# Performance work log

Measured on AMD Instinct MI355X. Metric: run time of the kernel, lower is better.

The kernel has to match this reference:

```python
import jax, jax.numpy as jnp
import numpy as np

B, H, W, C, NH, WS, NB = 8, 64, 64, 384, 12, 8, 2
N = H * W
NWT = WS * WS  # tokens per window
SHIFT = WS // 2

def _rel_index(ws):
    coords = np.stack(np.meshgrid(np.arange(ws), np.arange(ws), indexing='ij')).reshape(2, -1)
    rel = (coords[:, :, None] - coords[:, None, :]).transpose(1, 2, 0)
    rel[..., 0] += ws - 1
    rel[..., 1] += ws - 1
    rel[..., 0] *= 2 * ws - 1
    return rel.sum(-1)  # (ws*ws, ws*ws)

REL_IDX = _rel_index(WS)

def _shift_mask(h, w, ws, shift):
    img = np.zeros((h, w))
    cnt = 0
    for hs in (slice(0, -ws), slice(-ws, -shift), slice(-shift, None)):
        for wsl in (slice(0, -ws), slice(-ws, -shift), slice(-shift, None)):
            img[hs, wsl] = cnt
            cnt += 1
    win = img.reshape(h // ws, ws, w // ws, ws).transpose(0, 2, 1, 3).reshape(-1, ws * ws)
    diff = win[:, None, :] - win[:, :, None]
    return np.where(diff != 0, -100.0, 0.0).astype(np.float32)  # (nW, NWT, NWT)

MASK = jnp.asarray(_shift_mask(H, W, WS, SHIFT))

def _ln(x, g, b, eps=1e-5):
    m = jnp.mean(x, -1, keepdims=True)
    v = jnp.mean((x - m) ** 2, -1, keepdims=True)
    return (x - m) * jax.lax.rsqrt(v + eps) * g + b

def _partition(x):
    b = x.shape[0]
    x = x.reshape(b, H // WS, WS, W // WS, WS, C).transpose(0, 1, 3, 2, 4, 5)
    return x.reshape(-1, NWT, C)

def _reverse(wx, b):
    x = wx.reshape(b, H // WS, W // WS, WS, WS, C).transpose(0, 1, 3, 2, 4, 5)
    return x.reshape(b, H, W, C)

def _attention(xw, qkv_w, qkv_b, proj_w, proj_b, rpb, mask):
    B_, Nt, Cc = xw.shape
    hd = Cc // NH
    qkv = (xw @ qkv_w + qkv_b).reshape(B_, Nt, 3, NH, hd).transpose(2, 0, 3, 1, 4)
    q, k, v = qkv[0], qkv[1], qkv[2]
    bias = rpb[REL_IDX].transpose(2, 0, 1)[None]  # (1, NH, Nt, Nt)
    attn = jnp.einsum('bhnd,bhmd->bhnm', q * (hd ** -0.5), k) + bias
    if mask is not None:
        nW = mask.shape[0]
        attn = attn.reshape(B_ // nW, nW, NH, Nt, Nt) + mask[None, :, None]
        attn = attn.reshape(B_, NH, Nt, Nt)
    attn = jax.nn.softmax(attn, axis=-1)
    out = jnp.einsum('bhnm,bhmd->bhnd', attn, v).transpose(0, 2, 1, 3).reshape(B_, Nt, Cc)
    return out @ proj_w + proj_b

def _swin_block(x, p, shift):
    n1g, n1b, n2g, n2b, qw, qb, pw, pb, w1, b1, w2, b2, rpb = p
    shortcut = x
    h = _ln(x, n1g, n1b)
    if shift > 0:
        h = jnp.roll(h, (-shift, -shift), axis=(1, 2))
    hw = _attention(_partition(h), qw, qb, pw, pb, rpb, MASK if shift > 0 else None)
    h = _reverse(hw, x.shape[0])
    if shift > 0:
        h = jnp.roll(h, (shift, shift), axis=(1, 2))
    x = shortcut + h
    h = _ln(x, n2g, n2b)
    h = jax.nn.gelu(h @ w1 + b1) @ w2 + b2
    return x + h


def setup_inputs() -> dict:
    key = jax.random.key(0)
    ks = jax.random.split(key, 6)
    s = 0.02
    return {
        'x': jax.random.normal(ks[0], (B, N, C), jnp.float32),
        'outer_g': jnp.ones((NB, C), jnp.float32),
        'outer_b': jnp.zeros((NB, C), jnp.float32),
        'n1_g': jnp.ones((NB, C), jnp.float32),
        'n1_b': jnp.zeros((NB, C), jnp.float32),
        'n2_g': jnp.ones((NB, C), jnp.float32),
        'n2_b': jnp.zeros((NB, C), jnp.float32),
        'qkv_w': jax.random.normal(ks[1], (NB, C, 3 * C), jnp.float32) * s,
        'qkv_b': jnp.zeros((NB, 3 * C), jnp.float32),
        'proj_w': jax.random.normal(ks[2], (NB, C, C), jnp.float32) * s,
        'proj_b': jnp.zeros((NB, C), jnp.float32),
        'mlp_w1': jax.random.normal(ks[3], (NB, C, 4 * C), jnp.float32) * s,
        'mlp_b1': jnp.zeros((NB, 4 * C), jnp.float32),
        'mlp_w2': jax.random.normal(ks[4], (NB, 4 * C, C), jnp.float32) * s,
        'mlp_b2': jnp.zeros((NB, C), jnp.float32),
        'rpb': jax.random.normal(ks[5], (NB, (2 * WS - 1) ** 2, NH), jnp.float32) * s,
    }


def reference(x, outer_g, outer_b, n1_g, n1_b, n2_g, n2_b, qkv_w, qkv_b, proj_w, proj_b, mlp_w1, mlp_b1, mlp_w2, mlp_b2, rpb):
    xv = x.reshape(B, H, W, C)
    for i in range(NB):
        shift = 0 if i % 2 == 0 else SHIFT
        p = (n1_g[i], n1_b[i], n2_g[i], n2_b[i], qkv_w[i], qkv_b[i], proj_w[i], proj_b[i],
             mlp_w1[i], mlp_b1[i], mlp_w2[i], mlp_b2[i], rpb[i])
        residual = xv
        xv = _swin_block(_ln(xv, outer_g[i], outer_b[i]), p, shift) + residual
    return xv.reshape(B, N, C)
```

## Files before the change

### kernel.cpp

```cpp
#include <hip/hip_runtime.h>
#include <hip/hip_bf16.h>

#define BATCH 8
#define HDIM 64
#define WDIM 64
#define CC 384
#define NHE 12
#define HD 32
#define NTOK 32768
#define NBLK 2

typedef short short8 __attribute__((ext_vector_type(8)));
typedef float f32x4 __attribute__((ext_vector_type(4)));

__device__ __forceinline__ float bf2f(unsigned short u) {
  return __uint_as_float(((unsigned int)u) << 16);
}
__device__ __forceinline__ unsigned short f2bf(float f) {
  __hip_bfloat16 h = __float2bfloat16(f);
  return *reinterpret_cast<unsigned short*>(&h);
}
__device__ __forceinline__ float wave_sum(float s) {
#pragma unroll
  for (int o = 32; o; o >>= 1) s += __shfl_xor(s, o, 64);
  return s;
}
__device__ __forceinline__ float gelu_f(float x) {
  float y = 0.7978845608028654f * (x + 0.044715f * x * x * x);
  float t = 1.0f - 2.0f / (__expf(2.0f * y) + 1.0f);
  return 0.5f * x * (1.0f + t);
}
__device__ __forceinline__ int regid(int x) {
  return x < 56 ? 0 : (x < 60 ? 1 : 2);
}
__device__ __forceinline__ void gload16(const void* g, void* l) {
  __builtin_amdgcn_global_load_lds(
      (const __attribute__((address_space(1))) unsigned int*)g,
      (__attribute__((address_space(3))) unsigned int*)l, 16, 0, 0);
}

__global__ __launch_bounds__(256) void wconv_all_kernel(
    const float* __restrict__ qkvw, const float* __restrict__ pw,
    const float* __restrict__ w1, const float* __restrict__ w2,
    unsigned short* __restrict__ wt) {
  int t = blockIdx.x;
  const int i = t / 432;
  t -= i * 432;
  unsigned short* wq = wt + (size_t)i * 1769472;
  const float* src;
  unsigned short* dst;
  int K, N, nx;
  if (t < 108)      { src = qkvw + (size_t)i * 442368; dst = wq;           K = 384;  N = 1152; nx = 18; }
  else if (t < 144) { t -= 108; src = pw + (size_t)i * 147456; dst = wq + 442368;  K = 384;  N = 384;  nx = 6; }
  else if (t < 288) { t -= 144; src = w1 + (size_t)i * 589824; dst = wq + 589824;  K = 384;  N = 1536; nx = 24; }
  else              { t -= 288; src = w2 + (size_t)i * 589824; dst = wq + 1179648; K = 1536; N = 384;  nx = 6; }
  const int bn = (t % nx) * 64, bk = (t / nx) * 64;
  __shared__ float tile[64 * 65];
  const int tt = threadIdx.x;
  const int lk = tt >> 2, ln = (tt & 3) * 16;
  const float* ps = src + (size_t)(bk + lk) * N + bn + ln;
#pragma unroll
  for (int j = 0; j < 4; ++j)
    *(float4*)&tile[lk * 65 + ln + 4 * j] = *(const float4*)(ps + 4 * j);
  __syncthreads();
  const int on = tt >> 2, ok = (tt & 3) * 16;
  unsigned short ob[16];
#pragma unroll
  for (int j = 0; j < 16; ++j) ob[j] = f2bf(tile[(ok + j) * 65 + on]);
  uint4* pd = (uint4*)(dst + (size_t)(bn + on) * K + bk + ok);
  pd[0] = ((const uint4*)ob)[0];
  pd[1] = ((const uint4*)ob)[1];
}

__global__ __launch_bounds__(256) void bias_prep_kernel(
    const float* __restrict__ rpb, float* __restrict__ biasT) {
  int idx = blockIdx.x * 256 + threadIdx.x;
  int m = idx & 63;
  int n = (idx >> 6) & 63;
  int h = idx >> 12;
  int dr = (n >> 3) - (m >> 3) + 7;
  int dc = (n & 7) - (m & 7) + 7;
  biasT[idx] = rpb[(dr * 15 + dc) * NHE + h];
}

__global__ __launch_bounds__(256) void ln_fused_kernel(
    const float* __restrict__ xin, const float* __restrict__ og,
    const float* __restrict__ ob, const float* __restrict__ n1g,
    const float* __restrict__ n1b, unsigned short* __restrict__ y0h,
    unsigned short* __restrict__ abuf, int shift) {
  const int lane = threadIdx.x & 63;
  const int token = blockIdx.x * 4 + (threadIdx.x >> 6);
  const float* px = xin + (size_t)token * CC;
  float v[6];
#pragma unroll
  for (int j = 0; j < 6; ++j) v[j] = px[j * 64 + lane];
  float s = 0.f;
#pragma unroll
  for (int j = 0; j < 6; ++j) s += v[j];
  s = wave_sum(s);
  float mean = s * (1.0f / CC);
  float q = 0.f;
#pragma unroll
  for (int j = 0; j < 6; ++j) { float d = v[j] - mean; q += d * d; }
  q = wave_sum(q);
  float rstd = rsqrtf(q * (1.0f / CC) + 1e-5f);
  unsigned short* py = y0h + (size_t)token * CC;
#pragma unroll
  for (int j = 0; j < 6; ++j) {
    int d = j * 64 + lane;
    float y = (v[j] - mean) * rstd * og[d] + ob[d];
    py[d] = f2bf(y);
    v[j] = y;
  }
  s = 0.f;
#pragma unroll
  for (int j = 0; j < 6; ++j) s += v[j];
  s = wave_sum(s);
  float mean2 = s * (1.0f / CC);
  q = 0.f;
#pragma unroll
  for (int j = 0; j < 6; ++j) { float d = v[j] - mean2; q += d * d; }
  q = wave_sum(q);
  float rstd2 = rsqrtf(q * (1.0f / CC) + 1e-5f);
  int b = token >> 12;
  int hh = (token >> 6) & 63;
  int ww = token & 63;
  int r = (hh - shift) & 63;
  int c = (ww - shift) & 63;
  int wrow = (((b << 6) + ((r >> 3) << 3) + (c >> 3)) << 6) + ((r & 7) << 3) + (c & 7);
  unsigned short* pa = abuf + (size_t)wrow * CC;
#pragma unroll
  for (int j = 0; j < 6; ++j) {
    int d = j * 64 + lane;
    pa[d] = f2bf((v[j] - mean2) * rstd2 * n1g[d] + n1b[d]);
  }
}

__global__ __launch_bounds__(256, 1) void apl_kernel(
    const unsigned short* __restrict__ qkv, const float* __restrict__ biasT,
    const unsigned short* __restrict__ y0h, const unsigned short* __restrict__ Btp,
    const float* __restrict__ pb, const float* __restrict__ g2,
    const float* __restrict__ b2, unsigned short* __restrict__ x1h,
    unsigned short* __restrict__ abuf, int shift) {
  __shared__ __align__(1024) char smem[65536];
  const int tid = threadIdx.x;
  const int wv = tid >> 6;
  const int lane = tid & 63;
  const int l0 = lane & 15;
  const int q = lane >> 4;
  const int wi = blockIdx.x;
  const int use_mask = (shift != 0);

  unsigned short* P16 = (unsigned short*)(smem + wv * 12288);
  unsigned short* Vt16 = (unsigned short*)(smem + wv * 12288 + 8192);
  float* Ol = (float*)(smem + wv * 12288);
  unsigned short* Obuf = (unsigned short*)(smem + 49152);

#define LDS_FENCE() asm volatile("s_waitcnt lgkmcnt(0)" ::: "memory")
#define LDS_BARRIER() do { LDS_FENCE(); __builtin_amdgcn_s_barrier(); } while (0)

#define LOADP(PP, KD, QD, VD)                                                          \
  {                                                                                    \
    const unsigned short* qb_ = qkv + (size_t)(wi * 64) * 1152 + (4 * (PP) + wv) * HD; \
    _Pragma("unroll") for (int mt_ = 0; mt_ < 4; ++mt_)                                \
        KD[mt_] = *(const short8*)(qb_ + (size_t)(16 * mt_ + l0) * 1152 + CC + 8 * q); \
    _Pragma("unroll") for (int nt_ = 0; nt_ < 4; ++nt_)                                \
        QD[nt_] = *(const short8*)(qb_ + (size_t)(16 * nt_ + l0) * 1152 + 8 * q);      \
    const uint4* pv_ = (const uint4*)(qb_ + (size_t)lane * 1152 + 2 * CC);             \
    VD[0] = pv_[0]; VD[1] = pv_[1]; VD[2] = pv_[2]; VD[3] = pv_[3];                    \
  }

  f32x4 pacc[4][6] = {};

  short8 kf[4], qf[4];
  uint4 varr4[4];
  LOADP(0, kf, qf, varr4);

  for (int p = 0; p < 3; ++p) {
    const int h = 4 * p + wv;

    {
      const unsigned short* varr = (const unsigned short*)varr4;
#pragma unroll
      for (int d = 0; d < 32; ++d)
        Vt16[d * 64 + 8 * ((lane >> 3) ^ (d & 7)) + (lane & 7)] = varr[d];
    }

    f32x4 acc[4][4];
    const float* bh = biasT + h * 4096;
#pragma unroll
    for (int mt = 0; mt < 4; ++mt)
#pragma unroll
      for (int nt = 0; nt < 4; ++nt)
        acc[mt][nt] = *(const f32x4*)(bh + (l0 + 16 * nt) * 64 + 16 * mt + 4 * q);

    short8 kfn[4], qfn[4];
    uint4 varrn[4];
    if (p < 2) { LOADP(p + 1, kfn, qfn, varrn); }

    __builtin_amdgcn_s_setprio(1);
#pragma unroll
    for (int mt = 0; mt < 4; ++mt)
#pragma unroll
      for (int nt = 0; nt < 4; ++nt)
        acc[mt][nt] = __builtin_amdgcn_mfma_f32_16x16x32_bf16(kf[mt], qf[nt], acc[mt][nt], 0, 0, 0);
    __builtin_amdgcn_s_setprio(0);

    if (use_mask) {
      int wloc = wi & 63;
      int wy = (wloc >> 3) * 8, wx = (wloc & 7) * 8;
      int idn[4], idm[16];
#pragma unroll
      for (int nt = 0; nt < 4; ++nt) {
        int n = l0 + 16 * nt;
        idn[nt] = regid(wy + (n >> 3)) * 3 + regid(wx + (n & 7));
      }
#pragma unroll
      for (int mt = 0; mt < 4; ++mt)
#pragma unroll
        for (int r = 0; r < 4; ++r) {
          int m = 16 * mt + 4 * q + r;
          idm[mt * 4 + r] = regid(wy + (m >> 3)) * 3 + regid(wx + (m & 7));
        }
#pragma unroll
      for (int mt = 0; mt < 4; ++mt)
#pragma unroll
        for (int nt = 0; nt < 4; ++nt)
#pragma unroll
          for (int r = 0; r < 4; ++r)
            acc[mt][nt][r] += (idm[mt * 4 + r] == idn[nt]) ? 0.0f : -100.0f;
    }

    float inv[4];
#pragma unroll
    for (int nt = 0; nt < 4; ++nt) {
      float m0 = -1e30f;
#pragma unroll
      for (int mt = 0; mt < 4; ++mt)
#pragma unroll
        for (int r = 0; r < 4; ++r) m0 = fmaxf(m0, acc[mt][nt][r]);
      m0 = fmaxf(m0, __shfl_xor(m0, 16, 64));
      m0 = fmaxf(m0, __shfl_xor(m0, 32, 64));
      float s0 = 0.f;
#pragma unroll
      for (int mt = 0; mt < 4; ++mt)
#pragma unroll
        for (int r = 0; r < 4; ++r) {
          float e = __expf(acc[mt][nt][r] - m0);
          acc[mt][nt][r] = e;
          s0 += e;
        }
      s0 += __shfl_xor(s0, 16, 64);
      s0 += __shfl_xor(s0, 32, 64);
      inv[nt] = 1.0f / s0;
    }

#pragma unroll
    for (int mt = 0; mt < 4; ++mt)
#pragma unroll
      for (int nt = 0; nt < 4; ++nt) {
        unsigned int lo = (unsigned int)f2bf(acc[mt][nt][0] * inv[nt]) |
                          ((unsigned int)f2bf(acc[mt][nt][1] * inv[nt]) << 16);
        unsigned int hi = (unsigned int)f2bf(acc[mt][nt][2] * inv[nt]) |
                          ((unsigned int)f2bf(acc[mt][nt][3] * inv[nt]) << 16);
        unsigned int* dst = (unsigned int*)&P16[(l0 + 16 * nt) * 64 +
                                                8 * ((2 * mt + (q >> 1)) ^ (l0 & 7)) + 4 * (q & 1)];
        dst[0] = lo;
        dst[1] = hi;
      }
    LDS_FENCE();

    f32x4 oacc[4][2] = {};
    __builtin_amdgcn_s_setprio(1);
#pragma unroll
    for (int kt = 0; kt < 2; ++kt) {
      short8 pa[4], vb[2];
#pragma unroll
      for (int nt = 0; nt < 4; ++nt)
        pa[nt] = *(const short8*)&P16[(l0 + 16 * nt) * 64 + 8 * ((q + 4 * kt) ^ (l0 & 7))];
#pragma unroll
      for (int dt = 0; dt < 2; ++dt)
        vb[dt] = *(const short8*)&Vt16[(l0 + 16 * dt) * 64 + 8 * ((q + 4 * kt) ^ (l0 & 7))];
#pragma unroll
      for (int nt = 0; nt < 4; ++nt)
#pragma unroll
        for (int dt = 0; dt < 2; ++dt)
          oacc[nt][dt] = __builtin_amdgcn_mfma_f32_16x16x32_bf16(pa[nt], vb[dt], oacc[nt][dt], 0, 0, 0);
    }
    __builtin_amdgcn_s_setprio(0);
    LDS_FENCE();

#pragma unroll
    for (int nt = 0; nt < 4; ++nt)
#pragma unroll
      for (int dt = 0; dt < 2; ++dt)
#pragma unroll
        for (int r = 0; r < 4; ++r)
          Ol[(16 * nt + 4 * q + r) * 34 + l0 + 16 * dt] = oacc[nt][dt][r];
    LDS_FENCE();

    uint4 opack[4];
    int posv[4];
#pragma unroll
    for (int jj = 0; jj < 4; ++jj) {
      int c = 4 * wv + jj;
      posv[jj] = (c & 8) | ((c ^ lane) & 7);
      unsigned short tmp[8];
#pragma unroll
      for (int e = 0; e < 8; ++e) tmp[e] = f2bf(Ol[lane * 34 + jj * 8 + e]);
      opack[jj] = *(const uint4*)tmp;
    }
    LDS_BARRIER();
#pragma unroll
    for (int jj = 0; jj < 4; ++jj)
      *(uint4*)&Obuf[lane * 128 + posv[jj] * 8] = opack[jj];
    LDS_BARRIER();

#pragma unroll
    for (int kfl = 0; kfl < 4; ++kfl) {
      short8 a[4], b[6];
      int c2 = kfl * 4 + q;
      int pos2 = (c2 & 8) | ((c2 ^ l0) & 7);
#pragma unroll
      for (int mt = 0; mt < 4; ++mt)
        a[mt] = *(const short8*)&Obuf[(16 * mt + l0) * 128 + pos2 * 8];
#pragma unroll
      for (int nt = 0; nt < 6; ++nt)
        b[nt] = *(const short8*)(Btp + (size_t)(wv * 96 + nt * 16 + l0) * 384 +
                                 128 * p + 32 * kfl + 8 * q);
      __builtin_amdgcn_s_setprio(1);
#pragma unroll
      for (int mt = 0; mt < 4; ++mt)
#pragma unroll
        for (int nt = 0; nt < 6; ++nt)
          pacc[mt][nt] = __builtin_amdgcn_mfma_f32_16x16x32_bf16(a[mt], b[nt], pacc[mt][nt], 0, 0, 0);
      __builtin_amdgcn_s_setprio(0);
    }

    if (p < 2) {
#pragma unroll
      for (int j = 0; j < 4; ++j) {
        kf[j] = kfn[j];
        qf[j] = qfn[j];
        varr4[j] = varrn[j];
      }
    }
  }
  LDS_BARRIER();

  float pbv[6], g2v[6], b2v[6];
#pragma unroll
  for (int nt = 0; nt < 6; ++nt) {
    int col = wv * 96 + nt * 16 + l0;
    pbv[nt] = pb[col];
    g2v[nt] = g2[col];
    b2v[nt] = b2[col];
  }
  int dstrow[4][4];
#pragma unroll
  for (int mt = 0; mt < 4; ++mt)
#pragma unroll
    for (int rr = 0; rr < 4; ++rr) {
      int m = 16 * mt + 4 * q + rr;
      int grow = wi * 64 + m;
      int b_ = grow >> 12;
      int wl = (grow >> 6) & 63;
      int t = grow & 63;
      int rs = ((wl >> 3) << 3) + (t >> 3);
      int cs = ((wl & 7) << 3) + (t & 7);
      int hh = (rs + shift) & 63;
      int ww = (cs + shift) & 63;
      dstrow[mt][rr] = (((b_ << 6) + hh) << 6) + ww;
    }
#pragma unroll
  for (int mt = 0; mt < 4; ++mt)
#pragma unroll
    for (int nt = 0; nt < 6; ++nt)
#pragma unroll
      for (int rr = 0; rr < 4; ++rr) {
        size_t dst = (size_t)dstrow[mt][rr] * CC + wv * 96 + nt * 16 + l0;
        pacc[mt][nt][rr] += pbv[nt] + bf2f(y0h[dst]);
      }
  float* part = (float*)(smem + 49152);
  float* stats = (float*)(smem + 49152 + 2048);
#pragma unroll
  for (int mt = 0; mt < 4; ++mt)
#pragma unroll
    for (int rr = 0; rr < 4; ++rr) {
      float s = 0.f, ss = 0.f;
#pragma unroll
      for (int nt = 0; nt < 6; ++nt) {
        float v = pacc[mt][nt][rr];
        s += v;
        ss += v * v;
      }
#pragma unroll
      for (int o = 8; o; o >>= 1) {
        s += __shfl_xor(s, o, 64);
        ss += __shfl_xor(ss, o, 64);
      }
      if (l0 == 0) {
        int m = 16 * mt + 4 * q + rr;
        part[(m * 4 + wv) * 2] = s;
        part[(m * 4 + wv) * 2 + 1] = ss;
      }
    }
  LDS_BARRIER();
  if (tid < 64) {
    float s = 0.f, ss = 0.f;
#pragma unroll
    for (int w = 0; w < 4; ++w) {
      s += part[(tid * 4 + w) * 2];
      ss += part[(tid * 4 + w) * 2 + 1];
    }
    float mean = s * (1.0f / CC);
    float var = ss * (1.0f / CC) - mean * mean;
    stats[tid * 2] = mean;
    stats[tid * 2 + 1] = rsqrtf(var + 1e-5f);
  }
  LDS_BARRIER();
#pragma unroll
  for (int mt = 0; mt < 4; ++mt)
#pragma unroll
    for (int rr = 0; rr < 4; ++rr) {
      int m = 16 * mt + 4 * q + rr;
      float mean = stats[m * 2];
      float rstd = stats[m * 2 + 1];
#pragma unroll
      for (int nt = 0; nt < 6; ++nt) {
        float v = pacc[mt][nt][rr];
        size_t dst = (size_t)dstrow[mt][rr] * CC + wv * 96 + nt * 16 + l0;
        x1h[dst] = f2bf(v);
        abuf[dst] = f2bf((v - mean) * rstd * g2v[nt] + b2v[nt]);
      }
    }
#undef LOADP
#undef LDS_BARRIER
#undef LDS_FENCE
}

template <int EPI, int NN, int KK>
__global__ __launch_bounds__(256, 2) void gemm_kernel(
    const unsigned short* __restrict__ A, const unsigned short* __restrict__ Bt,
    const float* __restrict__ bias, float* __restrict__ outf,
    unsigned short* __restrict__ outb, const unsigned short* __restrict__ add0h,
    const float* __restrict__ add1f) {
  __shared__ __align__(1024) char smem[65536];
  const int tid = threadIdx.x;
  const int lane = tid & 63;
  const int wv = tid >> 6;
  const int wm = wv & 1, wn = wv >> 1;
  const int rowBase = blockIdx.y * 128;
  const int colBase = blockIdx.x * 128;
  const int srow = lane >> 3;
  const int schunk = (lane & 7) ^ srow;
  const unsigned short* pA = A + (size_t)(rowBase + srow) * KK + 8 * schunk;
  const unsigned short* pB = Bt + (size_t)(colBase + srow) * KK + 8 * schunk;
  const int l0 = lane & 15;
  const int q = lane >> 4;
  f32x4 acc[4][4] = {};

#pragma unroll
  for (int i = 0; i < 4; ++i) {
    int c = i * 4 + wv;
    gload16(pA + (size_t)(8 * c) * KK, smem + c * 1024);
    gload16(pB + (size_t)(8 * c) * KK, smem + 16384 + c * 1024);
  }

#pragma unroll 2
  for (int k0 = 0; k0 < KK; k0 += 64) {
    const int cur = (k0 >> 6) & 1;
    char* curb = smem + cur * 32768;
    if (k0 + 64 < KK) {
      char* nxtb = smem + (cur ^ 1) * 32768;
#pragma unroll
      for (int i = 0; i < 4; ++i) {
        int c = i * 4 + wv;
        gload16(pA + (size_t)(8 * c) * KK + k0 + 64, nxtb + c * 1024);
        gload16(pB + (size_t)(8 * c) * KK + k0 + 64, nxtb + 16384 + c * 1024);
      }
      asm volatile("s_waitcnt vmcnt(8)" ::: "memory");
    } else {
      asm volatile("s_waitcnt vmcnt(0)" ::: "memory");
    }
    __builtin_amdgcn_s_barrier();
    const unsigned short* As = (const unsigned short*)curb;
    const unsigned short* Bs = (const unsigned short*)(curb + 16384);
#pragma unroll
    for (int ksub = 0; ksub < 2; ++ksub) {
      const int sc = ksub * 4 + q;
      short8 af[4], bfr[4];
#pragma unroll
      for (int im = 0; im < 4; ++im) {
        int r = wm * 64 + im * 16 + l0;
        af[im] = *(const short8*)&As[r * 64 + 8 * (sc ^ (r & 7))];
      }
#pragma unroll
      for (int in_ = 0; in_ < 4; ++in_) {
        int r = wn * 64 + in_ * 16 + l0;
        bfr[in_] = *(const short8*)&Bs[r * 64 + 8 * (sc ^ (r & 7))];
      }
      __builtin_amdgcn_s_setprio(1);
#pragma unroll
      for (int im = 0; im < 4; ++im)
#pragma unroll
        for (int in_ = 0; in_ < 4; ++in_)
          acc[im][in_] = __builtin_amdgcn_mfma_f32_16x16x32_bf16(
              af[im], bfr[in_], acc[im][in_], 0, 0, 0);
      __builtin_amdgcn_s_setprio(0);
    }
    __builtin_amdgcn_s_barrier();
  }
  const int quad = lane >> 4;
  const int lc = lane & 15;
#pragma unroll
  for (int im = 0; im < 4; ++im) {
    int rb = rowBase + wm * 64 + im * 16 + quad * 4;
#pragma unroll
    for (int in_ = 0; in_ < 4; ++in_) {
      int gcol = colBase + wn * 64 + in_ * 16 + lc;
      float bv = bias[gcol];
#pragma unroll
      for (int r = 0; r < 4; ++r) {
        int grow = rb + r;
        float v = acc[im][in_][r] + bv;
        if (EPI == 0) {
          if (gcol < CC) v *= 0.17677669529663687f;
          outb[(size_t)grow * NN + gcol] = f2bf(v);
        } else if (EPI == 1) {
          outb[(size_t)grow * NN + gcol] = f2bf(gelu_f(v));
        } else {
          size_t dst = (size_t)grow * CC + gcol;
          outf[dst] = bf2f(add0h[dst]) + add1f[dst] + v;
        }
      }
    }
  }
}

extern "C" void kernel_launch(void* const* d_in, const int* in_sizes, int n_in,
                              void* d_out, int out_size, void* d_ws, size_t ws_size,
                              hipStream_t stream) {
  const float* x    = (const float*)d_in[0];
  const float* og   = (const float*)d_in[1];
  const float* ob   = (const float*)d_in[2];
  const float* n1g  = (const float*)d_in[3];
  const float* n1b  = (const float*)d_in[4];
  const float* n2g  = (const float*)d_in[5];
  const float* n2b  = (const float*)d_in[6];
  const float* qkvw = (const float*)d_in[7];
  const float* qkvb = (const float*)d_in[8];
  const float* pw   = (const float*)d_in[9];
  const float* pb   = (const float*)d_in[10];
  const float* w1   = (const float*)d_in[11];
  const float* b1   = (const float*)d_in[12];
  const float* w2   = (const float*)d_in[13];
  const float* b2   = (const float*)d_in[14];
  const float* rpb  = (const float*)d_in[15];
  float* out = (float*)d_out;

  char* ws = (char*)d_ws;
  unsigned short* y0h   = (unsigned short*)(ws);
  unsigned short* x1h   = (unsigned short*)(ws + 25165824);
  unsigned short* a_bf  = (unsigned short*)(ws + 50331648);
  unsigned short* big_bf= (unsigned short*)(ws + 100663296);
  unsigned short* wt    = (unsigned short*)(ws + 201326592);
  float* biasT          = (float*)(ws + 100663296 + 75497472);

  wconv_all_kernel<<<864, 256, 0, stream>>>(qkvw, pw, w1, w2, wt);

  for (int i = 0; i < NBLK; ++i) {
    const float* xin = (i == 0) ? x : out;
    int shift = (i & 1) ? 4 : 0;
    unsigned short* wq = wt + (size_t)i * 1769472;
    ln_fused_kernel<<<8192, 256, 0, stream>>>(xin, og + i * 384, ob + i * 384,
                                              n1g + i * 384, n1b + i * 384, y0h, a_bf, shift);
    gemm_kernel<0, 1152, 384><<<dim3(9, 256), 256, 0, stream>>>(
        a_bf, wq, qkvb + i * 1152, nullptr, big_bf, nullptr, nullptr);
    bias_prep_kernel<<<192, 256, 0, stream>>>(rpb + i * 2700, biasT);
    apl_kernel<<<512, 256, 0, stream>>>(big_bf, biasT, y0h, wq + 442368,
                                        pb + i * 384, n2g + i * 384, n2b + i * 384,
                                        x1h, a_bf, shift);
    gemm_kernel<1, 1536, 384><<<dim3(12, 256), 256, 0, stream>>>(
        a_bf, wq + 589824, b1 + i * 1536, nullptr, big_bf, nullptr, nullptr);
    gemm_kernel<3, 384, 1536><<<dim3(3, 256), 256, 0, stream>>>(
        big_bf, wq + 1179648, b2 + i * 384, out, nullptr, x1h, xin);
  }
}
```

Baseline: 702.8 us.

## Drop QKV register prefetch to double attention occupancy; remap GEMM tile order

The attention kernel stops prefetching the next head's Q/K/V fragments into registers and loads them at the start of each head iteration. This frees registers so the launch bound can request two blocks per CU, trading the explicit software prefetch for latency hiding through more resident waves. Separately, the GEMM kernel remaps its block index so groups of 8 consecutive blocks cover 8 row tiles of the same column tile, which is meant to improve L2 reuse of the B operand.

```diff
diff --git a/kernel.cpp b/kernel.cpp
--- a/kernel.cpp
+++ b/kernel.cpp
@@ -136,7 +136,7 @@
   }
 }
 
-__global__ __launch_bounds__(256, 1) void apl_kernel(
+__global__ __launch_bounds__(256, 2) void apl_kernel(
     const unsigned short* __restrict__ qkv, const float* __restrict__ biasT,
     const unsigned short* __restrict__ y0h, const unsigned short* __restrict__ Btp,
     const float* __restrict__ pb, const float* __restrict__ g2,
@@ -159,44 +159,36 @@
 #define LDS_FENCE() asm volatile("s_waitcnt lgkmcnt(0)" ::: "memory")
 #define LDS_BARRIER() do { LDS_FENCE(); __builtin_amdgcn_s_barrier(); } while (0)
 
-#define LOADP(PP, KD, QD, VD)                                                          \
-  {                                                                                    \
-    const unsigned short* qb_ = qkv + (size_t)(wi * 64) * 1152 + (4 * (PP) + wv) * HD; \
-    _Pragma("unroll") for (int mt_ = 0; mt_ < 4; ++mt_)                                \
-        KD[mt_] = *(const short8*)(qb_ + (size_t)(16 * mt_ + l0) * 1152 + CC + 8 * q); \
-    _Pragma("unroll") for (int nt_ = 0; nt_ < 4; ++nt_)                                \
-        QD[nt_] = *(const short8*)(qb_ + (size_t)(16 * nt_ + l0) * 1152 + 8 * q);      \
-    const uint4* pv_ = (const uint4*)(qb_ + (size_t)lane * 1152 + 2 * CC);             \
-    VD[0] = pv_[0]; VD[1] = pv_[1]; VD[2] = pv_[2]; VD[3] = pv_[3];                    \
-  }
-
   f32x4 pacc[4][6] = {};
-
-  short8 kf[4], qf[4];
-  uint4 varr4[4];
-  LOADP(0, kf, qf, varr4);
 
   for (int p = 0; p < 3; ++p) {
     const int h = 4 * p + wv;
+    const unsigned short* qbase = qkv + (size_t)(wi * 64) * 1152 + h * HD;
+    short8 kf[4], qf[4];
+#pragma unroll
+    for (int mt = 0; mt < 4; ++mt)
+      kf[mt] = *(const short8*)(qbase + (size_t)(16 * mt + l0) * 1152 + CC + 8 * q);
+#pragma unroll
+    for (int nt = 0; nt < 4; ++nt)
+      qf[nt] = *(const short8*)(qbase + (size_t)(16 * nt + l0) * 1152 + 8 * q);
+
+    f32x4 acc[4][4];
+    const float* bh = biasT + h * 4096;
+#pragma unroll
+    for (int mt = 0; mt < 4; ++mt)
+#pragma unroll
+      for (int nt = 0; nt < 4; ++nt)
+        acc[mt][nt] = *(const f32x4*)(bh + (l0 + 16 * nt) * 64 + 16 * mt + 4 * q);
 
     {
-      const unsigned short* varr = (const unsigned short*)varr4;
+      unsigned short varr[32];
+      const uint4* pv = (const uint4*)(qbase + (size_t)lane * 1152 + 2 * CC);
+      uint4* t4 = (uint4*)varr;
+      t4[0] = pv[0]; t4[1] = pv[1]; t4[2] = pv[2]; t4[3] = pv[3];
 #pragma unroll
       for (int d = 0; d < 32; ++d)
         Vt16[d * 64 + 8 * ((lane >> 3) ^ (d & 7)) + (lane & 7)] = varr[d];
     }
-
-    f32x4 acc[4][4];
-    const float* bh = biasT + h * 4096;
-#pragma unroll
-    for (int mt = 0; mt < 4; ++mt)
-#pragma unroll
-      for (int nt = 0; nt < 4; ++nt)
-        acc[mt][nt] = *(const f32x4*)(bh + (l0 + 16 * nt) * 64 + 16 * mt + 4 * q);
-
-    short8 kfn[4], qfn[4];
-    uint4 varrn[4];
-    if (p < 2) { LOADP(p + 1, kfn, qfn, varrn); }
 
     __builtin_amdgcn_s_setprio(1);
 #pragma unroll
@@ -335,15 +327,6 @@
         for (int nt = 0; nt < 6; ++nt)
           pacc[mt][nt] = __builtin_amdgcn_mfma_f32_16x16x32_bf16(a[mt], b[nt], pacc[mt][nt], 0, 0, 0);
       __builtin_amdgcn_s_setprio(0);
-    }
-
-    if (p < 2) {
-#pragma unroll
-      for (int j = 0; j < 4; ++j) {
-        kf[j] = kfn[j];
-        qf[j] = qfn[j];
-        varr4[j] = varrn[j];
-      }
     }
   }
   LDS_BARRIER();
@@ -434,7 +417,6 @@
         abuf[dst] = f2bf((v - mean) * rstd * g2v[nt] + b2v[nt]);
       }
     }
-#undef LOADP
 #undef LDS_BARRIER
 #undef LDS_FENCE
 }
@@ -450,8 +432,11 @@
   const int lane = tid & 63;
   const int wv = tid >> 6;
   const int wm = wv & 1, wn = wv >> 1;
-  const int rowBase = blockIdx.y * 128;
-  const int colBase = blockIdx.x * 128;
+  constexpr int NX = NN / 128;
+  const int f = blockIdx.y * NX + blockIdx.x;
+  const int g = f >> 3;
+  const int rowBase = ((f & 7) + 8 * (g / NX)) * 128;
+  const int colBase = (g % NX) * 128;
   const int srow = lane >> 3;
   const int schunk = (lane & 7) ^ srow;
   const unsigned short* pA = A + (size_t)(rowBase + srow) * KK + 8 * schunk;
```

Measured after the change: 608.5 us. -13.4%, faster.
